# Optimization experiments

Measured on AMD Instinct MI355X. Metric: run time of the kernel, lower is better.

## Reference

```python
import jax, jax.numpy as jnp
import numpy as np

K = 16
ITERS = 5
DIST_CHUNK = 8  # feature-chunk size to avoid materializing [B,F,S,S]


def pairwise_l1(x):
    """x: [B, F, S] -> d: [B, S, S], d[b,i,j] = ||x[b,:,i]-x[b,:,j]||_1.
    Computed in feature chunks via scan so peak intermediate is [B,CH,S,S]."""
    B, F, S = x.shape
    xc = x.reshape(B, F // DIST_CHUNK, DIST_CHUNK, S).transpose(1, 0, 2, 3)  # [F/CH,B,CH,S]

    def step(acc, blk):  # blk: [B, CH, S]
        return acc + jnp.abs(blk[:, :, :, None] - blk[:, :, None, :]).sum(axis=1), None

    d, _ = jax.lax.scan(step, jnp.zeros((B, S, S), x.dtype), xc)
    return d


def kmedoids_pool(x, w):
    B, F, S = x.shape
    wm = jnp.mean(w, axis=1)                       # [B,S] per-token attention weight
    d = pairwise_l1(x)                             # [B,S,S]
    _, ctr = jax.lax.top_k(wm, K)                  # [B,K] initial medoids
    dw = d * wm[:, None, :]                        # d[b,i,j]*w[b,j]
    for _ in range(ITERS):
        # distance from every token to each current medoid: [B,S,K]
        i2c = jnp.take_along_axis(d, jnp.broadcast_to(ctr[:, None, :], (B, S, K)), axis=2)
        assign = jnp.argmin(i2c, axis=2)           # [B,S] cluster assignment
        member = jax.nn.one_hot(assign, K, dtype=x.dtype)  # [B,S,K]
        # weighted within-cluster cost for candidate i in cluster k:
        # cost[b,i,k] = sum_j d[b,i,j]*w[b,j]*member[b,j,k]
        cost = jnp.einsum('bij,bjk->bik', dw, member)
        cost = jnp.where(member > 0, cost, jnp.inf)  # medoid must be a member
        ctr = jnp.argmin(cost, axis=1)             # [B,K] new medoids
    idx = jnp.broadcast_to(ctr[:, None, :], (B, F, K))
    return jnp.take_along_axis(x, idx, axis=2)     # [B,F,K]


def setup_inputs() -> dict:
    key = jax.random.key(0)
    kx, kw = jax.random.split(key)
    B, F, S = 8, 256, 1024
    x = jax.random.normal(kx, (B, F, S), dtype=jnp.float32)
    w = jax.random.uniform(kw, (B, S, S), dtype=jnp.float32)
    return {"x": x, "w": w}


def reference(x, w):
    return kmedoids_pool(x, w)
```

## Files before the change

kernel.cpp:

```cpp
#include <hip/hip_runtime.h>
#include <math.h>

#define BB 8
#define FF 256
#define SS 1024
#define KK 16
#define ITERS 5
#define NG 64

typedef unsigned long long ull;

__device__ __forceinline__ ull umin64(ull a, ull b) { return a < b ? a : b; }

#define FCD 8
__device__ __forceinline__ void async_copy16(const float* g, const float* s) {
    __builtin_amdgcn_global_load_lds((const __attribute__((address_space(1))) void*)g,
                                     (__attribute__((address_space(3))) void*)s, 16, 0, 0);
}

__global__ __launch_bounds__(128, 4) void dist_kernel(const float* __restrict__ x,
                                                      float* __restrict__ d,
                                                      const float* __restrict__ wfull,
                                                      float* __restrict__ wm) {
    int b = blockIdx.y;
    if (blockIdx.x >= 264) {
        int gthr = (blockIdx.x - 264) * 128 + threadIdx.x;
        const float* wb = wfull + (size_t)b * SS * SS;
#pragma unroll
        for (int h = 0; h < 2; ++h) {
            int j = gthr + h * 512;
            const float* col = wb + j;
            float tot = 0.f;
            for (int ic = 0; ic < 8; ++ic) {
                float p = 0.f;
#pragma unroll 16
                for (int i = 0; i < 128; ++i) p += col[(size_t)(ic * 128 + i) * SS];
                tot += p;
            }
            wm[b * SS + j] = tot * (1.0f / SS);
        }
        return;
    }
    __shared__ float smem[2048];
    int tid = threadIdx.x;
    int wave = tid >> 6, lane = tid & 63;
    int tw = blockIdx.x * 2 + wave;
    int it = 0, rem = tw;
    while (rem >= 32 - it) { rem -= 32 - it; ++it; }
    int jt = it + rem;
    int i0 = it * 32, j0 = jt * 32;
    const float* xb = x + (size_t)b * FF * SS;
    float* db = d + (size_t)b * SS * SS;
    float* wbase = smem + wave * 1024;
    int ly = lane >> 3, lx = lane & 7;
    int sFl = lane >> 3, sTk = (lane & 7) * 4;

    float acc[4][4] = {};

    auto stage = [&](int c, int h) {
        float* A = wbase + h * 512;
        const float* base = xb + (size_t)c * FCD * SS + (size_t)sFl * SS;
        async_copy16(base + i0 + sTk, A);
        async_copy16(base + j0 + sTk, A + 256);
    };
    auto compute = [&](int h) {
        const float* A = wbase + h * 512;
        const float* B = A + 256;
#pragma unroll
        for (int f = 0; f < FCD; ++f) {
            float4 a = *(const float4*)(A + f * 32 + ly * 4);
            float4 bb = *(const float4*)(B + f * 32 + lx * 4);
            float av[4] = {a.x, a.y, a.z, a.w};
            float bv[4] = {bb.x, bb.y, bb.z, bb.w};
#pragma unroll
            for (int r = 0; r < 4; ++r)
#pragma unroll
                for (int c = 0; c < 4; ++c)
                    acc[r][c] += fabsf(av[r] - bv[c]);
        }
    };

    stage(0, 0);
#pragma unroll 1
    for (int k = 0; k < FF / FCD - 1; ++k) {
        asm volatile("s_waitcnt lgkmcnt(0)" ::: "memory");
        stage(k + 1, (k + 1) & 1);
        asm volatile("s_waitcnt vmcnt(2)" ::: "memory");
        compute(k & 1);
    }
    asm volatile("s_waitcnt vmcnt(0)" ::: "memory");
    compute(1);

#pragma unroll
    for (int r = 0; r < 4; ++r) {
        float4 v = make_float4(acc[r][0], acc[r][1], acc[r][2], acc[r][3]);
        *(float4*)&db[(size_t)(i0 + ly * 4 + r) * SS + j0 + lx * 4] = v;
    }
    if (it != jt) {
#pragma unroll
        for (int c = 0; c < 4; ++c) {
            float4 v = make_float4(acc[0][c], acc[1][c], acc[2][c], acc[3][c]);
            *(float4*)&db[(size_t)(j0 + lx * 4 + c) * SS + i0 + ly * 4] = v;
        }
    }
}

__global__ __launch_bounds__(1024) void topk_kernel(const float* __restrict__ wm,
                                                    ull* __restrict__ part0) {
    int b = blockIdx.x;
    int tid = threadIdx.x;
    int lane = tid & 63, wv = tid >> 6;
    __shared__ ull red[16];
    __shared__ int ctr_s[KK];
    float v = wm[b * SS + tid];
    ull key = (((ull)__float_as_uint(v)) << 32) | (ull)(0xFFFFFFFFu - (unsigned)tid);
    for (int k = 0; k < KK; ++k) {
        ull kk = key;
#pragma unroll
        for (int off = 32; off; off >>= 1) {
            ull o = __shfl_down(kk, off, 64);
            if (o > kk) kk = o;
        }
        if (lane == 0) red[wv] = kk;
        __syncthreads();
        if (wv == 0) {
            ull k2 = (lane < 16) ? red[lane] : 0ull;
#pragma unroll
            for (int off = 8; off; off >>= 1) {
                ull o = __shfl_down(k2, off, 64);
                if (o > k2) k2 = o;
            }
            if (lane == 0) red[0] = k2;
        }
        __syncthreads();
        ull W = red[0];
        int widx = (int)(0xFFFFFFFFu - (unsigned)(W & 0xFFFFFFFFu));
        if (tid == widx) key = 0;
        if (tid == 0) ctr_s[k] = widx;
        __syncthreads();
    }
    int k = tid >> 6, g = tid & 63;
    part0[((size_t)b * KK + k) * NG + g] =
        (g == 0) ? (ull)(unsigned)ctr_s[k] : ~0ull;
}

__global__ __launch_bounds__(256) void iter_kernel(const float* __restrict__ d,
                                                   const float* __restrict__ wm,
                                                   const ull* __restrict__ pprev,
                                                   ull* __restrict__ pnext) {
    int b = blockIdx.y, g = blockIdx.x;
    int tid = threadIdx.x;
    int lane = tid & 63, wv = tid >> 6;
    __shared__ float wmv[SS];
    __shared__ int asg[SS];
    __shared__ int ctr_s[KK];
    __shared__ ull m16[KK][17];
    __shared__ ull rowkey[16];
    *(float4*)&wmv[tid * 4] = *(const float4*)&wm[b * SS + tid * 4];
    {
        int k = tid >> 4, s = tid & 15;
        const ull* pp = &pprev[((size_t)b * KK + k) * NG + s * 4];
        ull m = umin64(umin64(pp[0], pp[1]), umin64(pp[2], pp[3]));
        m16[k][s] = m;
    }
    __syncthreads();
    if (tid < KK) {
        ull m = m16[tid][0];
#pragma unroll
        for (int s = 1; s < 16; ++s) m = umin64(m, m16[tid][s]);
        ctr_s[tid] = (m == ~0ull) ? 0 : (int)(m & 0xFFFFFFFFu);
    }
    __syncthreads();
    const float* db = d + (size_t)b * SS * SS;
#pragma unroll
    for (int t = 0; t < 4; ++t) {
        int j = t * 256 + tid;
        ull bk = ~0ull;
#pragma unroll
        for (int k = 0; k < KK; ++k) {
            float vv = db[(size_t)ctr_s[k] * SS + j];
            ull key = (((ull)__float_as_uint(vv)) << 32) | (unsigned)k;
            if (key < bk) bk = key;
        }
        asg[j] = (int)(bk & 0xFFFFFFFFu);
    }
    __syncthreads();
#pragma unroll
    for (int r = 0; r < 4; ++r) {
        int i = g * 16 + wv * 4 + r;
        int my = asg[i];
        const float* drow = db + (size_t)i * SS;
        float s = 0.f;
#pragma unroll
        for (int c = 0; c < 4; ++c) {
            int j = c * 256 + lane * 4;
            float4 dv = *(const float4*)&drow[j];
            float4 w4 = *(const float4*)&wmv[j];
            int4 a4 = *(const int4*)&asg[j];
            s += (a4.x == my) ? dv.x * w4.x : 0.f;
            s += (a4.y == my) ? dv.y * w4.y : 0.f;
            s += (a4.z == my) ? dv.z * w4.z : 0.f;
            s += (a4.w == my) ? dv.w * w4.w : 0.f;
        }
#pragma unroll
        for (int off = 32; off; off >>= 1) s += __shfl_down(s, off, 64);
        if (lane == 0)
            rowkey[wv * 4 + r] = (((ull)__float_as_uint(s)) << 32) | (unsigned)i;
    }
    __syncthreads();
    if (tid < KK) {
        ull m = ~0ull;
#pragma unroll
        for (int r = 0; r < 16; ++r)
            if (asg[g * 16 + r] == tid) m = umin64(m, rowkey[r]);
        pnext[((size_t)b * KK + tid) * NG + g] = m;
    }
}

__global__ __launch_bounds__(256) void gather_kernel(const float* __restrict__ x,
                                                     const ull* __restrict__ pfin,
                                                     float* __restrict__ out) {
    int b = blockIdx.y, q = blockIdx.x;
    int tid = threadIdx.x;
    __shared__ ull m16[KK][17];
    __shared__ int ctr_s[KK];
    {
        int k = tid >> 4, s = tid & 15;
        const ull* pp = &pfin[((size_t)b * KK + k) * NG + s * 4];
        ull m = umin64(umin64(pp[0], pp[1]), umin64(pp[2], pp[3]));
        m16[k][s] = m;
    }
    __syncthreads();
    if (tid < KK) {
        ull m = m16[tid][0];
#pragma unroll
        for (int s = 1; s < 16; ++s) m = umin64(m, m16[tid][s]);
        ctr_s[tid] = (m == ~0ull) ? 0 : (int)(m & 0xFFFFFFFFu);
    }
    __syncthreads();
#pragma unroll
    for (int t = 0; t < 4; ++t) {
        int e = q * 1024 + t * 256 + tid;
        int f = e >> 4, k = e & 15;
        out[((size_t)b * FF + f) * KK + k] = x[((size_t)b * FF + f) * SS + ctr_s[k]];
    }
}

extern "C" void kernel_launch(void* const* d_in, const int* in_sizes, int n_in,
                              void* d_out, int out_size, void* d_ws, size_t ws_size,
                              hipStream_t stream) {
    const float* x = (const float*)d_in[0];
    const float* w = (const float*)d_in[1];
    float* out = (float*)d_out;

    char* ws = (char*)d_ws;
    float* d = (float*)ws;
    size_t off = (size_t)BB * SS * SS * sizeof(float);
    float* wm = (float*)(ws + off);   off += (size_t)BB * SS * sizeof(float);
    off = (off + 15) & ~(size_t)15;
    ull* part = (ull*)(ws + off);
    const size_t PST = (size_t)BB * KK * NG;

    dist_kernel<<<dim3(268, BB), 128, 0, stream>>>(x, d, w, wm);
    topk_kernel<<<BB, 1024, 0, stream>>>(wm, part);
    for (int t = 1; t <= ITERS; ++t)
        iter_kernel<<<dim3(NG, BB), 256, 0, stream>>>(d, wm, part + (t - 1) * PST,
                                                      part + t * PST);
    gather_kernel<<<dim3(4, BB), 256, 0, stream>>>(x, part + ITERS * PST, out);
}
```

Before: 241.5 us.

## Split w column-mean into separate partial-sum kernel, finish reduction in topk

Moves the mean-over-rows of w out of the extra dist_kernel blocks into a dedicated kernel that splits rows into 8 chunks across a 3D grid, writing partial sums. topk_kernel now sums the partials, scales, and writes wm. The goal is more parallelism on the 32MB w read, since the old path used only 4 blocks per batch with long serial column loops that could tail the distance kernel. It adds a kernel launch and a small partial buffer in the workspace.

```diff
diff --git a/kernel.cpp b/kernel.cpp
--- a/kernel.cpp
+++ b/kernel.cpp
@@ -12,6 +12,17 @@
 
 __device__ __forceinline__ ull umin64(ull a, ull b) { return a < b ? a : b; }
 
+#define ICH 8
+__global__ void wm_part_kernel(const float* __restrict__ w, float* __restrict__ part) {
+    int j = blockIdx.x * 256 + threadIdx.x;
+    int ic = blockIdx.y, b = blockIdx.z;
+    const float* wp = w + (size_t)b * SS * SS + (size_t)ic * (SS / ICH) * SS + j;
+    float s = 0.f;
+#pragma unroll 16
+    for (int i = 0; i < SS / ICH; ++i) s += wp[(size_t)i * SS];
+    part[((size_t)ic * BB + b) * SS + j] = s;
+}
+
 #define FCD 8
 __device__ __forceinline__ void async_copy16(const float* g, const float* s) {
     __builtin_amdgcn_global_load_lds((const __attribute__((address_space(1))) void*)g,
@@ -19,33 +30,13 @@
 }
 
 __global__ __launch_bounds__(128, 4) void dist_kernel(const float* __restrict__ x,
-                                                      float* __restrict__ d,
-                                                      const float* __restrict__ wfull,
-                                                      float* __restrict__ wm) {
+                                                      float* __restrict__ d) {
+    __shared__ float smem[2048];
+    int tid = threadIdx.x;
+    int wave = tid >> 6, lane = tid & 63;
     int b = blockIdx.y;
-    if (blockIdx.x >= 264) {
-        int gthr = (blockIdx.x - 264) * 128 + threadIdx.x;
-        const float* wb = wfull + (size_t)b * SS * SS;
-#pragma unroll
-        for (int h = 0; h < 2; ++h) {
-            int j = gthr + h * 512;
-            const float* col = wb + j;
-            float tot = 0.f;
-            for (int ic = 0; ic < 8; ++ic) {
-                float p = 0.f;
-#pragma unroll 16
-                for (int i = 0; i < 128; ++i) p += col[(size_t)(ic * 128 + i) * SS];
-                tot += p;
-            }
-            wm[b * SS + j] = tot * (1.0f / SS);
-        }
-        return;
-    }
-    __shared__ float smem[2048];
-    int tid = threadIdx.x;
-    int wave = tid >> 6, lane = tid & 63;
-    int tw = blockIdx.x * 2 + wave;
-    int it = 0, rem = tw;
+    int w = blockIdx.x * 2 + wave;
+    int it = 0, rem = w;
     while (rem >= 32 - it) { rem -= 32 - it; ++it; }
     int jt = it + rem;
     int i0 = it * 32, j0 = jt * 32;
@@ -105,14 +96,19 @@
     }
 }
 
-__global__ __launch_bounds__(1024) void topk_kernel(const float* __restrict__ wm,
+__global__ __launch_bounds__(1024) void topk_kernel(const float* __restrict__ wpart,
+                                                    float* __restrict__ wm,
                                                     ull* __restrict__ part0) {
     int b = blockIdx.x;
     int tid = threadIdx.x;
     int lane = tid & 63, wv = tid >> 6;
     __shared__ ull red[16];
     __shared__ int ctr_s[KK];
-    float v = wm[b * SS + tid];
+    float v = 0.f;
+#pragma unroll
+    for (int ic = 0; ic < ICH; ++ic) v += wpart[((size_t)ic * BB + b) * SS + tid];
+    v *= (1.0f / SS);
+    wm[b * SS + tid] = v;
     ull key = (((ull)__float_as_uint(v)) << 32) | (ull)(0xFFFFFFFFu - (unsigned)tid);
     for (int k = 0; k < KK; ++k) {
         ull kk = key;
@@ -256,13 +252,15 @@
     char* ws = (char*)d_ws;
     float* d = (float*)ws;
     size_t off = (size_t)BB * SS * SS * sizeof(float);
-    float* wm = (float*)(ws + off);   off += (size_t)BB * SS * sizeof(float);
+    float* wm = (float*)(ws + off);    off += (size_t)BB * SS * sizeof(float);
     off = (off + 15) & ~(size_t)15;
-    ull* part = (ull*)(ws + off);
+    ull* part = (ull*)(ws + off);      off += (size_t)(ITERS + 1) * BB * KK * NG * sizeof(ull);
+    float* wpart = (float*)(ws + off);
     const size_t PST = (size_t)BB * KK * NG;
 
-    dist_kernel<<<dim3(268, BB), 128, 0, stream>>>(x, d, w, wm);
-    topk_kernel<<<BB, 1024, 0, stream>>>(wm, part);
+    wm_part_kernel<<<dim3(SS / 256, ICH, BB), 256, 0, stream>>>(w, wpart);
+    dist_kernel<<<dim3(264, BB), 128, 0, stream>>>(x, d);
+    topk_kernel<<<BB, 1024, 0, stream>>>(wpart, wm, part);
     for (int t = 1; t <= ITERS; ++t)
         iter_kernel<<<dim3(NG, BB), 256, 0, stream>>>(d, wm, part + (t - 1) * PST,
                                                       part + t * PST);
```

Measured after the change: 235.4 us. 2.5% less time.
